# Performance work log

Hardware: AMD Instinct MI355X
Metric: run time of the kernel (lower is better)

The kernel has to match this reference:

```python
import jax, jax.numpy as jnp
import numpy as np
from jax import lax

B, T, D = 64, 1024, 256   # batch, seq_len, input_size
H, C = 1024, 1000         # hidden_size, num_classes


def setup_inputs() -> dict:
    key = jax.random.key(0)
    k_x, k_ih, k_hh, k_b, k_fc, k_fb = jax.random.split(key, 6)
    x = jax.random.normal(k_x, (B, T, D), dtype=jnp.float32)
    # scaled init so the 1024-step recurrence stays numerically sane
    w_ih = jax.random.normal(k_ih, (H, D), dtype=jnp.float32) * (1.0 / np.sqrt(D))
    w_hh = jax.random.normal(k_hh, (H, H), dtype=jnp.float32) * (0.5 / np.sqrt(H))
    b_mod = jax.random.normal(k_b, (H,), dtype=jnp.float32) * 0.01 - 0.1
    w_fc = jax.random.normal(k_fc, (C, H), dtype=jnp.float32) * (1.0 / np.sqrt(H))
    b_fc = jnp.zeros((C,), dtype=jnp.float32)
    return {"x": x, "w_ih": w_ih, "w_hh": w_hh, "b_mod": b_mod,
            "w_fc": w_fc, "b_fc": b_fc}


def reference(x, w_ih, w_hh, b_mod, w_fc, b_fc):
    # modReLU RNN: h_t = sign(z_t) * relu(|z_t| + b),  z_t = W_ih x_t + W_hh h_{t-1}
    # fc head applied to last hidden state (out[:, -1, :]).
    bsz = x.shape[0]
    # precompute input projections for all timesteps: [B, T, H]
    xproj = jnp.einsum('btd,hd->bth', x, w_ih)

    def step(h, x_t):
        z = x_t + h @ w_hh.T                      # [B, H]
        h_new = jnp.sign(z) * jnp.maximum(jnp.abs(z) + b_mod, 0.0)
        return h_new, None

    h0 = jnp.zeros((bsz, w_hh.shape[0]), dtype=x.dtype)
    h_last, _ = lax.scan(step, h0, jnp.swapaxes(xproj, 0, 1))  # scan over T
    return h_last @ w_fc.T + b_fc  # [B, C]
```

## Files before the change

kernel.cpp:

```cpp
#include <hip/hip_runtime.h>

typedef __bf16 bf16;
typedef __bf16 bf16x4 __attribute__((ext_vector_type(4)));
typedef __bf16 bf16x8 __attribute__((ext_vector_type(8)));
typedef float f32x4 __attribute__((ext_vector_type(4)));
typedef unsigned long long u64;
typedef unsigned int u32;

#define T_STEPS 1024
#define BATCH   64
#define DIN     256
#define HID     1024
#define NBLK    128
#define RING    8
#define FSTRIDE 32

__global__ __launch_bounds__(256) void xproj_gemm(
    const float* __restrict__ x, const float* __restrict__ w_ih,
    bf16* __restrict__ xproj)
{
    __shared__ bf16 As[128 * 40];
    __shared__ bf16 Bs[128 * 40];
    const int tid = threadIdx.x;
    const int m0 = blockIdx.x * 128;
    const int n0 = blockIdx.y * 128;
    const int w = tid >> 6, lane = tid & 63;
    const int r = lane & 15, q = lane >> 4;

    f32x4 acc[2][8];
    #pragma unroll
    for (int i = 0; i < 2; i++)
        #pragma unroll
        for (int j = 0; j < 8; j++)
            acc[i][j] = (f32x4){0.f, 0.f, 0.f, 0.f};

    for (int kk = 0; kk < 8; kk++) {
        const int k0 = kk * 32;
        __syncthreads();
        #pragma unroll
        for (int j = 0; j < 4; j++) {
            int u = tid + j * 256;
            int row = u >> 3, c4 = u & 7;
            float4 fa = *(const float4*)&x[(size_t)(m0 + row) * DIN + k0 + c4 * 4];
            bf16x4 va = { (bf16)fa.x, (bf16)fa.y, (bf16)fa.z, (bf16)fa.w };
            *(bf16x4*)&As[row * 40 + c4 * 4] = va;
            float4 fb = *(const float4*)&w_ih[(size_t)(n0 + row) * DIN + k0 + c4 * 4];
            bf16x4 vb = { (bf16)fb.x, (bf16)fb.y, (bf16)fb.z, (bf16)fb.w };
            *(bf16x4*)&Bs[row * 40 + c4 * 4] = vb;
        }
        __syncthreads();
        bf16x8 a0 = *(const bf16x8*)&As[(w * 32 + r) * 40 + q * 8];
        bf16x8 a1 = *(const bf16x8*)&As[(w * 32 + 16 + r) * 40 + q * 8];
        #pragma unroll
        for (int nt = 0; nt < 8; nt++) {
            bf16x8 bb = *(const bf16x8*)&Bs[(nt * 16 + r) * 40 + q * 8];
            acc[0][nt] = __builtin_amdgcn_mfma_f32_16x16x32_bf16(a0, bb, acc[0][nt], 0, 0, 0);
            acc[1][nt] = __builtin_amdgcn_mfma_f32_16x16x32_bf16(a1, bb, acc[1][nt], 0, 0, 0);
        }
    }

    #pragma unroll
    for (int mi = 0; mi < 2; mi++)
        #pragma unroll
        for (int nt = 0; nt < 8; nt++)
            #pragma unroll
            for (int reg = 0; reg < 4; reg++) {
                int gm = m0 + w * 32 + mi * 16 + q * 4 + reg;
                int n  = n0 + nt * 16 + r;
                int b  = gm >> 10, t = gm & 1023;
                xproj[(((t << 6) + b) << 10) + n] = (bf16)acc[mi][nt][reg];
            }
}

__global__ __launch_bounds__(512) void rnn_rec(
    const float* __restrict__ w_hh, const float* __restrict__ b_mod,
    const bf16* __restrict__ xproj, u64* __restrict__ hbuf,
    float* __restrict__ hT, u32* __restrict__ flags)
{
    __shared__ bf16 Wl[16 * 1032];
    __shared__ float Red[2][6 * 288];

    const int tid = threadIdx.x;
    const int f0 = (int)(blockIdx.x >> 1) * 16;
    const int fg = (int)(blockIdx.x >> 1);
    const int half = (int)(blockIdx.x & 1);
    const int b0 = half * 32;
    const int w = tid >> 6, lane = tid & 63;
    const int r = lane & 15, q = lane >> 4;
    const int bg = w & 1, kq = w >> 1;
    const int batchA = b0 + bg * 16 + r;

    #pragma unroll
    for (int j = 0; j < 8; j++) {
        int u = tid + j * 512;
        int row = u >> 8, c4 = u & 255;
        float4 f = *(const float4*)&w_hh[(size_t)(f0 + row) * HID + c4 * 4];
        bf16x4 v = { (bf16)f.x, (bf16)f.y, (bf16)f.z, (bf16)f.w };
        *(bf16x4*)&Wl[row * 1032 + c4 * 4] = v;
    }
    const float bc = b_mod[f0 + r];
    __syncthreads();

    const int wkBase = r * 1032 + kq * 256 + q * 8;
    bf16x8 Bf[8];
    #pragma unroll
    for (int ks = 0; ks < 8; ks++)
        Bf[ks] = *(const bf16x8*)&Wl[wkBase + ks * 32];

    u32* hbuf32 = (u32*)hbuf;
    const int dom = (half << 1) + bg;
    u32* pollFlag = flags + (size_t)(dom * 64 + kq * 16 + r) * FSTRIDE;
    u32* pubFlag  = flags + (size_t)(dom * 64 + fg) * FSTRIDE;

    float xpv[4];
    if (kq == 0) {
        #pragma unroll
        for (int reg = 0; reg < 4; reg++) {
            int b = b0 + bg * 16 + q * 4 + reg;
            xpv[reg] = (float)xproj[(b << 10) + f0 + r];
        }
    }

    for (int t = 0; t < T_STEPS; t++) {
        const int rp = t & (RING - 1), wp = (t + 1) & (RING - 1);

        const u32 tgt = (u32)t;
        for (;;) {
            u32 f = __hip_atomic_load(pollFlag, __ATOMIC_RELAXED, __HIP_MEMORY_SCOPE_AGENT);
            if (__all((int)(f >= tgt))) break;
        }

        const u64* H = hbuf + (size_t)rp * 16384 + batchA * 256 + kq * 64 + q * 2;
        union { u64 u[2]; bf16x8 v; } A[8];
        #pragma unroll
        for (int ks = 0; ks < 8; ks++) {
            A[ks].u[0] = __hip_atomic_load(&H[ks*8    ], __ATOMIC_RELAXED, __HIP_MEMORY_SCOPE_AGENT);
            A[ks].u[1] = __hip_atomic_load(&H[ks*8 + 1], __ATOMIC_RELAXED, __HIP_MEMORY_SCOPE_AGENT);
        }

        f32x4 acc0 = {0.f,0.f,0.f,0.f}, acc1 = {0.f,0.f,0.f,0.f};
        #pragma unroll
        for (int ks = 0; ks < 8; ks += 2) {
            acc0 = __builtin_amdgcn_mfma_f32_16x16x32_bf16(A[ks].v,     Bf[ks],     acc0, 0, 0, 0);
            acc1 = __builtin_amdgcn_mfma_f32_16x16x32_bf16(A[ks + 1].v, Bf[ks + 1], acc1, 0, 0, 0);
        }

        if (kq > 0) {
            const int slot = ((kq - 1) * 2 + bg) * 288;
            #pragma unroll
            for (int reg = 0; reg < 4; reg++)
                Red[t & 1][slot + (q * 4 + reg) * 18 + r] = acc0[reg] + acc1[reg];
        }
        __syncthreads();

        if (kq == 0) {
            float hv4[4];
            #pragma unroll
            for (int reg = 0; reg < 4; reg++) {
                float z = acc0[reg] + acc1[reg];
                #pragma unroll
                for (int p = 0; p < 3; p++)
                    z += Red[t & 1][(p * 2 + bg) * 288 + (q * 4 + reg) * 18 + r];
                z += xpv[reg];
                hv4[reg] = copysignf(fmaxf(fabsf(z) + bc, 0.0f), z);
            }
            if (t == T_STEPS - 1) {
                #pragma unroll
                for (int reg = 0; reg < 4; reg++)
                    hT[(f0 + r) * 64 + b0 + bg * 16 + q * 4 + reg] = hv4[reg];
            } else {
                #pragma unroll
                for (int reg = 0; reg < 4; reg++) {
                    const int b = b0 + bg * 16 + q * 4 + reg;
                    float other = __shfl_xor(hv4[reg], 1);
                    if ((r & 1) == 0) {
                        u32 lo = (u32)__builtin_bit_cast(unsigned short, (bf16)hv4[reg]);
                        u32 hi = (u32)__builtin_bit_cast(unsigned short, (bf16)other);
                        __hip_atomic_store(&hbuf32[(size_t)wp * 32768 + (b << 9) + ((f0 + r) >> 1)],
                                           lo | (hi << 16), __ATOMIC_RELAXED, __HIP_MEMORY_SCOPE_AGENT);
                    }
                }
                asm volatile("s_waitcnt vmcnt(0)" ::: "memory");
                if (lane == 0)
                    __hip_atomic_store(pubFlag, (u32)(t + 1), __ATOMIC_RELAXED, __HIP_MEMORY_SCOPE_AGENT);
                #pragma unroll
                for (int reg = 0; reg < 4; reg++) {
                    int b = b0 + bg * 16 + q * 4 + reg;
                    xpv[reg] = (float)xproj[((size_t)(t + 1) << 16) + (b << 10) + f0 + r];
                }
            }
        }
    }
}

__global__ __launch_bounds__(256) void fc_head(
    const float* __restrict__ hT, const float* __restrict__ w_fc,
    const float* __restrict__ b_fc, float* __restrict__ out)
{
    const int tid = threadIdx.x;
    const int b = tid & 63;
    const int c = blockIdx.x * 4 + (tid >> 6);
    float acc = b_fc[c];
    #pragma unroll 8
    for (int k = 0; k < HID; k++)
        acc = fmaf(hT[k * 64 + b], w_fc[(size_t)c * HID + k], acc);
    out[b * 1000 + c] = acc;
}

extern "C" void kernel_launch(void* const* d_in, const int* in_sizes, int n_in,
                              void* d_out, int out_size, void* d_ws, size_t ws_size,
                              hipStream_t stream)
{
    const float* x     = (const float*)d_in[0];
    const float* w_ih  = (const float*)d_in[1];
    const float* w_hh  = (const float*)d_in[2];
    const float* b_mod = (const float*)d_in[3];
    const float* w_fc  = (const float*)d_in[4];
    const float* b_fc  = (const float*)d_in[5];
    float* out = (float*)d_out;

    char* ws = (char*)d_ws;
    bf16*  xproj = (bf16*)ws;
    u64*   hbuf  = (u64*)(ws + 134217728);
    float* hT    = (float*)(ws + 134217728 + 1048576);
    u32*   flags = (u32*)(ws + 134217728 + 1048576 + 262144);

    hipMemsetAsync(hbuf, 0, 131072, stream);
    hipMemsetAsync(flags, 0, 256 * FSTRIDE * 4, stream);

    dim3 g1(512, 8);
    xproj_gemm<<<g1, 256, 0, stream>>>(x, w_ih, xproj);
    rnn_rec<<<NBLK, 512, 0, stream>>>(w_hh, b_mod, xproj, hbuf, hT, flags);
    fc_head<<<250, 256, 0, stream>>>(hT, w_fc, b_fc, out);
}
```

Measured before the change: 5.997 ms.

## Shrink recurrent grid to 32 blocks, each owning 64 hidden features

The persistent recurrence kernel now runs 32 blocks instead of 128. Each block holds 64 rows of W_hh in LDS and registers and computes four 16-feature tiles per wave. The k-split partial sums are exchanged through a reduce-scatter in LDS, so every wave finalizes and publishes its own 16 features, where before one wave did the epilogue. The aim is fewer participants in the cross-block flag synchronization each step and better use of each CU, at the cost of roughly four times more MFMA work per block per step, a larger LDS footprint near the 160KB limit, more registers, and an extra __syncthreads per step.

```diff
diff --git a/kernel.cpp b/kernel.cpp
--- a/kernel.cpp
+++ b/kernel.cpp
@@ -11,7 +11,7 @@
 #define BATCH   64
 #define DIN     256
 #define HID     1024
-#define NBLK    128
+#define NBLK    32
 #define RING    8
 #define FSTRIDE 32
 
@@ -72,53 +72,52 @@
             }
 }
 
-__global__ __launch_bounds__(512) void rnn_rec(
+__global__ __launch_bounds__(512, 2) void rnn_rec(
     const float* __restrict__ w_hh, const float* __restrict__ b_mod,
     const bf16* __restrict__ xproj, u64* __restrict__ hbuf,
     float* __restrict__ hT, u32* __restrict__ flags)
 {
-    __shared__ bf16 Wl[16 * 1032];
-    __shared__ float Red[2][6 * 288];
+    __shared__ bf16 Wl[64 * 1032];
+    __shared__ float Red[24 * 272];
 
     const int tid = threadIdx.x;
-    const int f0 = (int)(blockIdx.x >> 1) * 16;
-    const int fg = (int)(blockIdx.x >> 1);
+    const int fg2 = (int)(blockIdx.x >> 1);
     const int half = (int)(blockIdx.x & 1);
+    const int f0 = fg2 * 64;
     const int b0 = half * 32;
     const int w = tid >> 6, lane = tid & 63;
     const int r = lane & 15, q = lane >> 4;
     const int bg = w & 1, kq = w >> 1;
     const int batchA = b0 + bg * 16 + r;
 
-    #pragma unroll
-    for (int j = 0; j < 8; j++) {
+    for (int j = 0; j < 32; j++) {
         int u = tid + j * 512;
         int row = u >> 8, c4 = u & 255;
         float4 f = *(const float4*)&w_hh[(size_t)(f0 + row) * HID + c4 * 4];
         bf16x4 v = { (bf16)f.x, (bf16)f.y, (bf16)f.z, (bf16)f.w };
         *(bf16x4*)&Wl[row * 1032 + c4 * 4] = v;
     }
-    const float bc = b_mod[f0 + r];
+    const int myF = f0 + kq * 16 + r;
+    const float bc = b_mod[myF];
     __syncthreads();
 
-    const int wkBase = r * 1032 + kq * 256 + q * 8;
-    bf16x8 Bf[8];
-    #pragma unroll
-    for (int ks = 0; ks < 8; ks++)
-        Bf[ks] = *(const bf16x8*)&Wl[wkBase + ks * 32];
+    bf16x8 Bf[4][8];
+    #pragma unroll
+    for (int nt = 0; nt < 4; nt++)
+        #pragma unroll
+        for (int ks = 0; ks < 8; ks++)
+            Bf[nt][ks] = *(const bf16x8*)&Wl[(nt * 16 + r) * 1032 + kq * 256 + ks * 32 + q * 8];
 
     u32* hbuf32 = (u32*)hbuf;
     const int dom = (half << 1) + bg;
     u32* pollFlag = flags + (size_t)(dom * 64 + kq * 16 + r) * FSTRIDE;
-    u32* pubFlag  = flags + (size_t)(dom * 64 + fg) * FSTRIDE;
+    u32* pubFlag  = flags + (size_t)(dom * 64 + fg2 * 4 + kq) * FSTRIDE;
 
     float xpv[4];
-    if (kq == 0) {
-        #pragma unroll
-        for (int reg = 0; reg < 4; reg++) {
-            int b = b0 + bg * 16 + q * 4 + reg;
-            xpv[reg] = (float)xproj[(b << 10) + f0 + r];
-        }
+    #pragma unroll
+    for (int reg = 0; reg < 4; reg++) {
+        int b = b0 + bg * 16 + q * 4 + reg;
+        xpv[reg] = (float)xproj[(b << 10) + myF];
     }
 
     for (int t = 0; t < T_STEPS; t++) {
@@ -138,56 +137,61 @@
             A[ks].u[1] = __hip_atomic_load(&H[ks*8 + 1], __ATOMIC_RELAXED, __HIP_MEMORY_SCOPE_AGENT);
         }
 
-        f32x4 acc0 = {0.f,0.f,0.f,0.f}, acc1 = {0.f,0.f,0.f,0.f};
-        #pragma unroll
-        for (int ks = 0; ks < 8; ks += 2) {
-            acc0 = __builtin_amdgcn_mfma_f32_16x16x32_bf16(A[ks].v,     Bf[ks],     acc0, 0, 0, 0);
-            acc1 = __builtin_amdgcn_mfma_f32_16x16x32_bf16(A[ks + 1].v, Bf[ks + 1], acc1, 0, 0, 0);
-        }
-
-        if (kq > 0) {
-            const int slot = ((kq - 1) * 2 + bg) * 288;
+        f32x4 acc[4];
+        #pragma unroll
+        for (int nt = 0; nt < 4; nt++) acc[nt] = (f32x4){0.f,0.f,0.f,0.f};
+        #pragma unroll
+        for (int ks = 0; ks < 8; ks++)
+            #pragma unroll
+            for (int nt = 0; nt < 4; nt++)
+                acc[nt] = __builtin_amdgcn_mfma_f32_16x16x32_bf16(A[ks].v, Bf[nt][ks], acc[nt], 0, 0, 0);
+
+        #pragma unroll
+        for (int nt = 0; nt < 4; nt++) {
+            if (nt == kq) continue;
+            const int s = (kq - nt - 1) & 3;
+            const int base = ((bg * 4 + nt) * 3 + s) * 272;
             #pragma unroll
             for (int reg = 0; reg < 4; reg++)
-                Red[t & 1][slot + (q * 4 + reg) * 18 + r] = acc0[reg] + acc1[reg];
-        }
-        __syncthreads();
-
-        if (kq == 0) {
-            float hv4[4];
+                Red[base + (q * 4 + reg) * 17 + r] = acc[nt][reg];
+        }
+        __syncthreads();
+
+        float hv4[4];
+        #pragma unroll
+        for (int reg = 0; reg < 4; reg++) {
+            float z = acc[kq][reg];
+            #pragma unroll
+            for (int s = 0; s < 3; s++)
+                z += Red[((bg * 4 + kq) * 3 + s) * 272 + (q * 4 + reg) * 17 + r];
+            z += xpv[reg];
+            hv4[reg] = copysignf(fmaxf(fabsf(z) + bc, 0.0f), z);
+        }
+        __syncthreads();
+
+        if (t == T_STEPS - 1) {
+            #pragma unroll
+            for (int reg = 0; reg < 4; reg++)
+                hT[myF * 64 + b0 + bg * 16 + q * 4 + reg] = hv4[reg];
+        } else {
             #pragma unroll
             for (int reg = 0; reg < 4; reg++) {
-                float z = acc0[reg] + acc1[reg];
-                #pragma unroll
-                for (int p = 0; p < 3; p++)
-                    z += Red[t & 1][(p * 2 + bg) * 288 + (q * 4 + reg) * 18 + r];
-                z += xpv[reg];
-                hv4[reg] = copysignf(fmaxf(fabsf(z) + bc, 0.0f), z);
+                const int b = b0 + bg * 16 + q * 4 + reg;
+                float other = __shfl_xor(hv4[reg], 1);
+                if ((r & 1) == 0) {
+                    u32 lo = (u32)__builtin_bit_cast(unsigned short, (bf16)hv4[reg]);
+                    u32 hi = (u32)__builtin_bit_cast(unsigned short, (bf16)other);
+                    __hip_atomic_store(&hbuf32[(size_t)wp * 32768 + (b << 9) + (myF >> 1)],
+                                       lo | (hi << 16), __ATOMIC_RELAXED, __HIP_MEMORY_SCOPE_AGENT);
+                }
             }
-            if (t == T_STEPS - 1) {
-                #pragma unroll
-                for (int reg = 0; reg < 4; reg++)
-                    hT[(f0 + r) * 64 + b0 + bg * 16 + q * 4 + reg] = hv4[reg];
-            } else {
-                #pragma unroll
-                for (int reg = 0; reg < 4; reg++) {
-                    const int b = b0 + bg * 16 + q * 4 + reg;
-                    float other = __shfl_xor(hv4[reg], 1);
-                    if ((r & 1) == 0) {
-                        u32 lo = (u32)__builtin_bit_cast(unsigned short, (bf16)hv4[reg]);
-                        u32 hi = (u32)__builtin_bit_cast(unsigned short, (bf16)other);
-                        __hip_atomic_store(&hbuf32[(size_t)wp * 32768 + (b << 9) + ((f0 + r) >> 1)],
-                                           lo | (hi << 16), __ATOMIC_RELAXED, __HIP_MEMORY_SCOPE_AGENT);
-                    }
-                }
-                asm volatile("s_waitcnt vmcnt(0)" ::: "memory");
-                if (lane == 0)
-                    __hip_atomic_store(pubFlag, (u32)(t + 1), __ATOMIC_RELAXED, __HIP_MEMORY_SCOPE_AGENT);
-                #pragma unroll
-                for (int reg = 0; reg < 4; reg++) {
-                    int b = b0 + bg * 16 + q * 4 + reg;
-                    xpv[reg] = (float)xproj[((size_t)(t + 1) << 16) + (b << 10) + f0 + r];
-                }
+            asm volatile("s_waitcnt vmcnt(0)" ::: "memory");
+            if (lane == 0)
+                __hip_atomic_store(pubFlag, (u32)(t + 1), __ATOMIC_RELAXED, __HIP_MEMORY_SCOPE_AGENT);
+            #pragma unroll
+            for (int reg = 0; reg < 4; reg++) {
+                int b = b0 + bg * 16 + q * 4 + reg;
+                xpv[reg] = (float)xproj[((size_t)(t + 1) << 16) + (b << 10) + myF];
             }
         }
     }
```

Measured after the change: 6.329 ms. 5.5% more time.
